# Optimization experiments

Hardware: AMD Instinct MI355X
Metric: run time of the kernel (lower is better)

The kernel has to match this reference:

```python
import jax, jax.numpy as jnp
import numpy as np

B, N, F_NODE, F_EDGE, F_G = 2, 512, 128, 16, 128
MID, OUT = 128, 128


def _linear_params(key, fan_in, fan_out):
    kw, kb = jax.random.split(key)
    scale = 1.0 / np.sqrt(fan_in)
    W = jax.random.normal(kw, (fan_in, fan_out), dtype=jnp.float32) * scale
    b = jnp.zeros((fan_out,), dtype=jnp.float32)
    return W, b


def setup_inputs() -> dict:
    key = jax.random.key(0)
    ks = jax.random.split(key, 12)
    features = jax.random.normal(ks[0], (B, N, F_NODE), dtype=jnp.float32)
    e_features = jax.random.normal(ks[1], (B, N, N, F_EDGE), dtype=jnp.float32)
    g_features = jax.random.normal(ks[2], (B, F_G), dtype=jnp.float32)
    adj = jax.random.randint(ks[3], (B, N, N), 0, 2).astype(jnp.float32)
    W1, b1 = _linear_params(ks[4], F_NODE, MID)
    W2, b2 = _linear_params(ks[5], F_NODE, MID)
    We, be = _linear_params(ks[6], F_EDGE, MID)
    Wg, bg = _linear_params(ks[7], F_G, MID)
    Wo1, bo1 = _linear_params(ks[8], F_NODE, OUT)
    Wo2, bo2 = _linear_params(ks[9], MID, OUT)
    return dict(features=features, e_features=e_features, g_features=g_features,
                adj=adj, W1=W1, b1=b1, W2=W2, b2=b2, We=We, be=be, Wg=Wg, bg=bg,
                Wo1=Wo1, bo1=bo1, Wo2=Wo2, bo2=bo2)


def reference(features, e_features, g_features, adj,
              W1, b1, W2, b2, We, be, Wg, bg, Wo1, bo1, Wo2, bo2):
    # Linear projections (haiku Linear = xW + b)
    msg_1 = jnp.einsum('bnf,fm->bnm', features, W1) + b1      # (b,n,mid)
    msg_2 = jnp.einsum('bnf,fm->bnm', features, W2) + b2      # (b,n,mid)
    msg_e = jnp.einsum('bije,em->bijm', e_features, We) + be  # (b,n,n,mid)
    msg_g = jnp.einsum('bg,gm->bm', g_features, Wg) + bg      # (b,mid)
    # All-pairs broadcast sum: (b,n,n,mid)
    msgs = (msg_1[:, None, :, :] + msg_2[:, :, None, :]
            + msg_e + msg_g[:, None, None, :])
    # Masked max reduction over axis=1 (default reduction=jnp.max)
    msgs = jnp.max(msgs * adj[..., None], axis=1)             # (b,n,mid)
    h_1 = jnp.einsum('bnf,fo->bno', features, Wo1) + bo1
    h_2 = jnp.einsum('bnm,mo->bno', msgs, Wo2) + bo2
    return h_1 + h_2
```

## Files before the change

### kernel.cpp

```cpp
#include <hip/hip_runtime.h>
#include <hip/hip_bf16.h>
#include <math.h>

#define B_   2
#define N_   512
#define FN   128
#define FE   16
#define MID_ 128

typedef __attribute__((ext_vector_type(8)))  short short8_t;
typedef __attribute__((ext_vector_type(16))) float f32x16;

__device__ __forceinline__ short f2bf(float f) {
    __bf16 h = (__bf16)f;
    return __builtin_bit_cast(short, h);
}

__global__ __launch_bounds__(64) void kA(
    const float* __restrict__ feat, const float* __restrict__ gfeat,
    const float* __restrict__ W1, const float* __restrict__ b1,
    const float* __restrict__ W2, const float* __restrict__ be,
    const float* __restrict__ Wg, const float* __restrict__ bg,
    const float* __restrict__ Wo1,
    float* __restrict__ msg1c, float* __restrict__ msg2, float* __restrict__ h1,
    float* __restrict__ msgg)
{
    const int bid = blockIdx.x;
    const int t   = threadIdx.x;

    if (bid >= 384) {
        const int b = bid - 384;
        const float* gb = gfeat + b * FN;
        #pragma unroll
        for (int half = 0; half < 2; ++half) {
            const int m = t + 64 * half;
            float mg = b1[m] + be[m] + bg[m];
            for (int k0 = 0; k0 < FN; k0 += 16) {
                float wv[16];
                #pragma unroll
                for (int u = 0; u < 16; ++u) wv[u] = Wg[(k0 + u) * MID_ + m];
                #pragma unroll
                for (int u = 0; u < 16; ++u) mg += gb[k0 + u] * wv[u];
            }
            msgg[b * MID_ + m] = mg;
        }
        return;
    }

    const int bb  = bid / 192;
    const int rem = bid - bb * 192;
    const int nt  = rem / 12;
    const int ct  = rem - nt * 12;
    const int w   = ct >> 2;
    const int c0  = (ct & 3) * 32;
    const int n0  = nt * 32;
    const int g   = t >> 5, lm = t & 31;

    const float* Ws  = (w == 0) ? W1    : (w == 1) ? W2   : Wo1;
    float*       dst = (w == 0) ? msg1c : (w == 1) ? msg2 : h1;

    short8_t Af[8];
    #pragma unroll
    for (int ks = 0; ks < 8; ++ks) {
        const float* ap = feat + (size_t)(bb * N_ + n0 + lm) * FN + ks * 16 + 8 * g;
        const float4 a0 = *(const float4*)ap;
        const float4 a1 = *(const float4*)(ap + 4);
        short8_t A;
        A[0] = f2bf(a0.x); A[1] = f2bf(a0.y); A[2] = f2bf(a0.z); A[3] = f2bf(a0.w);
        A[4] = f2bf(a1.x); A[5] = f2bf(a1.y); A[6] = f2bf(a1.z); A[7] = f2bf(a1.w);
        Af[ks] = A;
    }
    short8_t Bfr[8];
    #pragma unroll
    for (int ks = 0; ks < 8; ++ks) {
        short8_t Bv;
        #pragma unroll
        for (int j = 0; j < 8; ++j)
            Bv[j] = f2bf(Ws[(size_t)(ks * 16 + 8 * g + j) * MID_ + c0 + lm]);
        Bfr[ks] = Bv;
    }

    f32x16 acc;
    #pragma unroll
    for (int r = 0; r < 16; ++r) acc[r] = 0.0f;
    #pragma unroll
    for (int ks = 0; ks < 8; ++ks)
        acc = __builtin_amdgcn_mfma_f32_32x32x16_bf16(Af[ks], Bfr[ks], acc, 0, 0, 0);

    #pragma unroll
    for (int r = 0; r < 16; ++r) {
        const int row = (r & 3) + 8 * (r >> 2) + 4 * g;
        dst[(size_t)(bb * N_ + n0 + row) * MID_ + c0 + lm] = acc[r];
    }
}

__global__ __launch_bounds__(512, 4) void kB(
    const float* __restrict__ ef, const float* __restrict__ adj,
    const float* __restrict__ We, const float* __restrict__ b2,
    const float* __restrict__ msg1c, const float* __restrict__ msg2,
    const float* __restrict__ msgg,
    float* __restrict__ part)
{
    __shared__ float    m2l[32 * MID_];
    __shared__ float    mtile[4][32 * 32];
    __shared__ unsigned madj[32];
    __shared__ float    anyzf[32];

    const int bid = blockIdx.x;
    const int b   = bid >> 8;
    const int jt  = (bid >> 4) & 15;
    const int ic  = bid & 15;
    const int j0  = jt * 32, i0 = ic * 32;
    const int t    = threadIdx.x;
    const int lane = t & 63, wid = t >> 6;
    const int mt   = wid & 3, ih = wid >> 2;
    const int g    = lane >> 5, lm = lane & 31;

    {
        const float4* src = (const float4*)(msg2 + (size_t)(b * N_ + i0) * MID_);
        ((float4*)m2l)[t]       = src[t];
        ((float4*)m2l)[t + 512] = src[t + 512];
    }
    #pragma unroll
    for (int p = 0; p < 2; ++p) {
        const int i_l = wid * 4 + 2 * p + g;
        const float av = adj[(size_t)(b * N_ + i0 + i_l) * N_ + j0 + lm];
        const unsigned long long bal = __ballot(av != 0.0f);
        if (lane == 0)  madj[wid * 4 + 2 * p]     = (unsigned)bal;
        if (lane == 32) madj[wid * 4 + 2 * p + 1] = (unsigned)(bal >> 32);
    }
    short8_t Bf;
    #pragma unroll
    for (int jj = 0; jj < 8; ++jj)
        Bf[jj] = f2bf(We[(8 * g + jj) * MID_ + mt * 32 + lm]);
    const float b2v = b2[mt * 32 + lm];

    f32x16 accm;
    #pragma unroll
    for (int r = 0; r < 16; ++r) accm[r] = -INFINITY;

    __syncthreads();

    if (t < 32) {
        unsigned ao = 0xFFFFFFFFu;
        #pragma unroll
        for (int i2 = 0; i2 < 32; ++i2) ao &= madj[i2];
        anyzf[t] = ((ao >> t) & 1u) ? -INFINITY : 0.0f;
    }

    const float* efr = ef + (((size_t)(b * N_ + i0 + ih * 16)) * N_ + j0 + lm) * FE + 8 * g;
    #pragma unroll 2
    for (int ii = 0; ii < 16; ++ii) {
        const int i_l = ih * 16 + ii;
        const float4 ea = *(const float4*)efr;
        const float4 eb = *(const float4*)(efr + 4);
        efr += (size_t)N_ * FE;
        short8_t Af;
        Af[0] = f2bf(ea.x); Af[1] = f2bf(ea.y); Af[2] = f2bf(ea.z); Af[3] = f2bf(ea.w);
        Af[4] = f2bf(eb.x); Af[5] = f2bf(eb.y); Af[6] = f2bf(eb.z); Af[7] = f2bf(eb.w);

        const unsigned vmg = madj[i_l] >> (4 * g);
        const float m2v = m2l[i_l * MID_ + mt * 32 + lm] + b2v;
        f32x16 C;
        #pragma unroll
        for (int r = 0; r < 16; ++r) {
            const int cr = (r & 3) + 8 * (r >> 2);
            C[r] = (vmg & (1u << cr)) ? m2v : -INFINITY;
        }
        const f32x16 S = __builtin_amdgcn_mfma_f32_32x32x16_bf16(Af, Bf, C, 0, 0, 0);
        #pragma unroll
        for (int r = 0; r < 16; ++r) accm[r] = fmaxf(accm[r], S[r]);
    }

    if (ih == 1) {
        #pragma unroll
        for (int r = 0; r < 16; ++r) {
            const int jrow = (r & 3) + 8 * (r >> 2) + 4 * g;
            mtile[mt][jrow * 32 + lm] = accm[r];
        }
    }
    __syncthreads();
    float* ftile = m2l;
    if (ih == 0) {
        #pragma unroll
        for (int r = 0; r < 16; ++r) {
            const int jrow = (r & 3) + 8 * (r >> 2) + 4 * g;
            ftile[jrow * MID_ + mt * 32 + lm] = fmaxf(accm[r], mtile[mt][jrow * 32 + lm]);
        }
    }
    __syncthreads();

    {
        const int jrow = t >> 4, m0 = (t & 15) * 8;
        const float az = anyzf[jrow];
        const float*  c1  = msg1c + (size_t)(b * N_ + j0 + jrow) * MID_ + m0;
        const float*  gg  = msgg + b * MID_ + m0;
        float*        dst = part  + ((size_t)(ic * 2 + b) * N_ + j0 + jrow) * MID_ + m0;
        const float*  tl  = &ftile[jrow * MID_ + m0];
        const float4 c1a = *(const float4*)c1;
        const float4 c1b = *(const float4*)(c1 + 4);
        const float4 g1a = *(const float4*)gg;
        const float4 g1b = *(const float4*)(gg + 4);
        float4 o0, o1;
        o0.x = fmaxf(tl[0] + c1a.x + g1a.x, az);
        o0.y = fmaxf(tl[1] + c1a.y + g1a.y, az);
        o0.z = fmaxf(tl[2] + c1a.z + g1a.z, az);
        o0.w = fmaxf(tl[3] + c1a.w + g1a.w, az);
        o1.x = fmaxf(tl[4] + c1b.x + g1b.x, az);
        o1.y = fmaxf(tl[5] + c1b.y + g1b.y, az);
        o1.z = fmaxf(tl[6] + c1b.z + g1b.z, az);
        o1.w = fmaxf(tl[7] + c1b.w + g1b.w, az);
        *(float4*)dst       = o0;
        *(float4*)(dst + 4) = o1;
    }
}

__global__ __launch_bounds__(256, 2) void kC(
    const float* __restrict__ part, const float* __restrict__ h1,
    const float* __restrict__ Wo2, const float* __restrict__ bo1,
    const float* __restrict__ bo2,
    float* __restrict__ out)
{
    __shared__ float ms[2 * MID_];
    const int bid = blockIdx.x;
    const int b   = bid >> 8;
    const int j0  = (bid & 255) * 2;
    const int t   = threadIdx.x;
    const int r   = t >> 7, m = t & 127;
    const size_t base = ((size_t)b * N_ + j0 + r) * MID_ + m;

    float u = -INFINITY;
    #pragma unroll
    for (int icc = 0; icc < 16; ++icc)
        u = fmaxf(u, part[(size_t)icc * 2 * N_ * MID_ + base]);
    ms[r * MID_ + m] = u;
    __syncthreads();

    float acc = h1[base] + bo1[m] + bo2[m];
    for (int k0 = 0; k0 < MID_; k0 += 8) {
        float wv[8];
        #pragma unroll
        for (int uu = 0; uu < 8; ++uu) wv[uu] = Wo2[(k0 + uu) * MID_ + m];
        #pragma unroll
        for (int uu = 0; uu < 8; ++uu) acc += ms[r * MID_ + k0 + uu] * wv[uu];
    }
    out[base] = acc;
}

extern "C" void kernel_launch(void* const* d_in, const int* in_sizes, int n_in,
                              void* d_out, int out_size, void* d_ws, size_t ws_size,
                              hipStream_t stream)
{
    const float* feat = (const float*)d_in[0];
    const float* ef   = (const float*)d_in[1];
    const float* gf   = (const float*)d_in[2];
    const float* adj  = (const float*)d_in[3];
    const float* W1   = (const float*)d_in[4];
    const float* b1   = (const float*)d_in[5];
    const float* W2   = (const float*)d_in[6];
    const float* b2   = (const float*)d_in[7];
    const float* We   = (const float*)d_in[8];
    const float* be   = (const float*)d_in[9];
    const float* Wg   = (const float*)d_in[10];
    const float* bg   = (const float*)d_in[11];
    const float* Wo1  = (const float*)d_in[12];
    const float* bo1  = (const float*)d_in[13];
    const float* Wo2  = (const float*)d_in[14];
    const float* bo2  = (const float*)d_in[15];
    float* out = (float*)d_out;

    float* ws    = (float*)d_ws;
    float* msg1c = ws;
    float* msg2  = ws + 131072;
    float* h1    = ws + 262144;
    float* part  = ws + 393216;
    float* msgg  = ws + 393216 + 2097152;

    hipLaunchKernelGGL(kA, dim3(386), dim3(64), 0, stream,
        feat, gf, W1, b1, W2, be, Wg, bg, Wo1, msg1c, msg2, h1, msgg);
    hipLaunchKernelGGL(kB, dim3(512), dim3(512), 0, stream,
        ef, adj, We, b2, msg1c, msg2, msgg, part);
    hipLaunchKernelGGL(kC, dim3(512), dim3(256), 0, stream,
        part, h1, Wo2, bo1, bo2, out);
}
```

Baseline: 30.07 us.

## Replace per-chunk partial buffer with atomicMax on order-preserving encoded floats

Instead of writing 16 partial max tiles to workspace and reducing them in kC, kB now combines results with atomicMax on an order-preserving unsigned encoding of the floats. kA zero-initialises the encoded buffer, and kC just decodes a single value. The edge-feature loop is also software-pipelined, loading the next row before processing the current one. This removes about 8MB of partial-buffer writes and reads, but adds many global atomics with contention across the 16 i-chunks, and the per-element stores are no longer vectorised.

```diff
diff --git a/kernel.cpp b/kernel.cpp
--- a/kernel.cpp
+++ b/kernel.cpp
@@ -14,6 +14,14 @@
 __device__ __forceinline__ short f2bf(float f) {
     __bf16 h = (__bf16)f;
     return __builtin_bit_cast(short, h);
+}
+__device__ __forceinline__ unsigned enc_f32(float f) {
+    unsigned u = __float_as_uint(f);
+    return u ^ (0x80000000u | (unsigned)((int)u >> 31));
+}
+__device__ __forceinline__ float dec_f32(unsigned u) {
+    unsigned m = (u & 0x80000000u) ? 0x80000000u : 0xFFFFFFFFu;
+    return __uint_as_float(u ^ m);
 }
 
 __global__ __launch_bounds__(64) void kA(
@@ -23,10 +31,21 @@
     const float* __restrict__ Wg, const float* __restrict__ bg,
     const float* __restrict__ Wo1,
     float* __restrict__ msg1c, float* __restrict__ msg2, float* __restrict__ h1,
-    float* __restrict__ msgg)
+    float* __restrict__ msgg, unsigned* __restrict__ msgs_enc)
 {
     const int bid = blockIdx.x;
     const int t   = threadIdx.x;
+
+    {
+        const int s0 = bid * 86;
+        #pragma unroll
+        for (int q = 0; q < 2; ++q) {
+            const int rel = t + 64 * q;
+            const int slot = s0 + rel;
+            if (rel < 86 && slot < 32768)
+                ((uint4*)msgs_enc)[slot] = make_uint4(0u, 0u, 0u, 0u);
+        }
+    }
 
     if (bid >= 384) {
         const int b = bid - 384;
@@ -99,7 +118,7 @@
     const float* __restrict__ We, const float* __restrict__ b2,
     const float* __restrict__ msg1c, const float* __restrict__ msg2,
     const float* __restrict__ msgg,
-    float* __restrict__ part)
+    unsigned* __restrict__ msgs_enc)
 {
     __shared__ float    m2l[32 * MID_];
     __shared__ float    mtile[4][32 * 32];
@@ -149,12 +168,18 @@
     }
 
     const float* efr = ef + (((size_t)(b * N_ + i0 + ih * 16)) * N_ + j0 + lm) * FE + 8 * g;
-    #pragma unroll 2
+    float4 ea = *(const float4*)efr;
+    float4 eb = *(const float4*)(efr + 4);
+    efr += (size_t)N_ * FE;
+    #pragma unroll
     for (int ii = 0; ii < 16; ++ii) {
+        float4 na, nb;
+        if (ii < 15) {
+            na = *(const float4*)efr;
+            nb = *(const float4*)(efr + 4);
+            efr += (size_t)N_ * FE;
+        }
         const int i_l = ih * 16 + ii;
-        const float4 ea = *(const float4*)efr;
-        const float4 eb = *(const float4*)(efr + 4);
-        efr += (size_t)N_ * FE;
         short8_t Af;
         Af[0] = f2bf(ea.x); Af[1] = f2bf(ea.y); Af[2] = f2bf(ea.z); Af[3] = f2bf(ea.w);
         Af[4] = f2bf(eb.x); Af[5] = f2bf(eb.y); Af[6] = f2bf(eb.z); Af[7] = f2bf(eb.w);
@@ -170,6 +195,7 @@
         const f32x16 S = __builtin_amdgcn_mfma_f32_32x32x16_bf16(Af, Bf, C, 0, 0, 0);
         #pragma unroll
         for (int r = 0; r < 16; ++r) accm[r] = fmaxf(accm[r], S[r]);
+        ea = na; eb = nb;
     }
 
     if (ih == 1) {
@@ -193,30 +219,20 @@
     {
         const int jrow = t >> 4, m0 = (t & 15) * 8;
         const float az = anyzf[jrow];
-        const float*  c1  = msg1c + (size_t)(b * N_ + j0 + jrow) * MID_ + m0;
-        const float*  gg  = msgg + b * MID_ + m0;
-        float*        dst = part  + ((size_t)(ic * 2 + b) * N_ + j0 + jrow) * MID_ + m0;
-        const float*  tl  = &ftile[jrow * MID_ + m0];
-        const float4 c1a = *(const float4*)c1;
-        const float4 c1b = *(const float4*)(c1 + 4);
-        const float4 g1a = *(const float4*)gg;
-        const float4 g1b = *(const float4*)(gg + 4);
-        float4 o0, o1;
-        o0.x = fmaxf(tl[0] + c1a.x + g1a.x, az);
-        o0.y = fmaxf(tl[1] + c1a.y + g1a.y, az);
-        o0.z = fmaxf(tl[2] + c1a.z + g1a.z, az);
-        o0.w = fmaxf(tl[3] + c1a.w + g1a.w, az);
-        o1.x = fmaxf(tl[4] + c1b.x + g1b.x, az);
-        o1.y = fmaxf(tl[5] + c1b.y + g1b.y, az);
-        o1.z = fmaxf(tl[6] + c1b.z + g1b.z, az);
-        o1.w = fmaxf(tl[7] + c1b.w + g1b.w, az);
-        *(float4*)dst       = o0;
-        *(float4*)(dst + 4) = o1;
+        const float*  c1 = msg1c + (size_t)(b * N_ + j0 + jrow) * MID_ + m0;
+        const float*  gg = msgg + b * MID_ + m0;
+        const float*  tl = &ftile[jrow * MID_ + m0];
+        unsigned* dst = msgs_enc + (size_t)(b * N_ + j0 + jrow) * MID_ + m0;
+        #pragma unroll
+        for (int q = 0; q < 8; ++q) {
+            const float v = fmaxf(tl[q] + c1[q] + gg[q], az);
+            atomicMax(dst + q, enc_f32(v));
+        }
     }
 }
 
 __global__ __launch_bounds__(256, 2) void kC(
-    const float* __restrict__ part, const float* __restrict__ h1,
+    const unsigned* __restrict__ msgs_enc, const float* __restrict__ h1,
     const float* __restrict__ Wo2, const float* __restrict__ bo1,
     const float* __restrict__ bo2,
     float* __restrict__ out)
@@ -229,11 +245,7 @@
     const int r   = t >> 7, m = t & 127;
     const size_t base = ((size_t)b * N_ + j0 + r) * MID_ + m;
 
-    float u = -INFINITY;
-    #pragma unroll
-    for (int icc = 0; icc < 16; ++icc)
-        u = fmaxf(u, part[(size_t)icc * 2 * N_ * MID_ + base]);
-    ms[r * MID_ + m] = u;
+    ms[r * MID_ + m] = dec_f32(msgs_enc[base]);
     __syncthreads();
 
     float acc = h1[base] + bo1[m] + bo2[m];
@@ -269,17 +281,17 @@
     const float* bo2  = (const float*)d_in[15];
     float* out = (float*)d_out;
 
-    float* ws    = (float*)d_ws;
-    float* msg1c = ws;
-    float* msg2  = ws + 131072;
-    float* h1    = ws + 262144;
-    float* part  = ws + 393216;
-    float* msgg  = ws + 393216 + 2097152;
+    float*    ws       = (float*)d_ws;
+    float*    msg1c    = ws;
+    float*    msg2     = ws + 131072;
+    float*    h1       = ws + 262144;
+    unsigned* msgs_enc = (unsigned*)(ws + 393216);
+    float*    msgg     = ws + 393216 + 131072;
 
     hipLaunchKernelGGL(kA, dim3(386), dim3(64), 0, stream,
-        feat, gf, W1, b1, W2, be, Wg, bg, Wo1, msg1c, msg2, h1, msgg);
+        feat, gf, W1, b1, W2, be, Wg, bg, Wo1, msg1c, msg2, h1, msgg, msgs_enc);
     hipLaunchKernelGGL(kB, dim3(512), dim3(512), 0, stream,
-        ef, adj, We, b2, msg1c, msg2, msgg, part);
+        ef, adj, We, b2, msg1c, msg2, msgg, msgs_enc);
     hipLaunchKernelGGL(kC, dim3(512), dim3(256), 0, stream,
-        part, h1, Wo2, bo1, bo2, out);
-}
+        msgs_enc, h1, Wo2, bo1, bo2, out);
+}
```

After: 75.50 us. 151% more time.

## Split waves over i into four groups each computing two M-tiles with shared A

Applied to the files above, without the earlier changes.

Changes the wave decomposition in kB: each wave now covers 64 output channels (two MFMA N-tiles) over 8 i-rows instead of 32 channels over 16 i-rows. The edge-feature load and bf16 conversion for A is reused across two MFMAs, halving per-wave global ef loads and conversions. In exchange it needs a two-level shared-memory tree reduction with an extra barrier, doubles the shared tile, and raises register pressure from two accumulators.

```diff
diff --git a/kernel.cpp b/kernel.cpp
--- a/kernel.cpp
+++ b/kernel.cpp
@@ -102,7 +102,7 @@
     float* __restrict__ part)
 {
     __shared__ float    m2l[32 * MID_];
-    __shared__ float    mtile[4][32 * 32];
+    __shared__ float    T[2][2][32 * 64];
     __shared__ unsigned madj[32];
     __shared__ float    anyzf[32];
 
@@ -113,7 +113,8 @@
     const int j0  = jt * 32, i0 = ic * 32;
     const int t    = threadIdx.x;
     const int lane = t & 63, wid = t >> 6;
-    const int mt   = wid & 3, ih = wid >> 2;
+    const int mtg  = wid >> 2;
+    const int ig   = wid & 3;
     const int g    = lane >> 5, lm = lane & 31;
 
     {
@@ -129,15 +130,18 @@
         if (lane == 0)  madj[wid * 4 + 2 * p]     = (unsigned)bal;
         if (lane == 32) madj[wid * 4 + 2 * p + 1] = (unsigned)(bal >> 32);
     }
-    short8_t Bf;
-    #pragma unroll
-    for (int jj = 0; jj < 8; ++jj)
-        Bf[jj] = f2bf(We[(8 * g + jj) * MID_ + mt * 32 + lm]);
-    const float b2v = b2[mt * 32 + lm];
-
-    f32x16 accm;
-    #pragma unroll
-    for (int r = 0; r < 16; ++r) accm[r] = -INFINITY;
+    short8_t Bf0, Bf1;
+    #pragma unroll
+    for (int jj = 0; jj < 8; ++jj) {
+        Bf0[jj] = f2bf(We[(8 * g + jj) * MID_ + mtg * 64 + lm]);
+        Bf1[jj] = f2bf(We[(8 * g + jj) * MID_ + mtg * 64 + 32 + lm]);
+    }
+    const float b2v0 = b2[mtg * 64 + lm];
+    const float b2v1 = b2[mtg * 64 + 32 + lm];
+
+    f32x16 accm0, accm1;
+    #pragma unroll
+    for (int r = 0; r < 16; ++r) { accm0[r] = -INFINITY; accm1[r] = -INFINITY; }
 
     __syncthreads();
 
@@ -148,10 +152,10 @@
         anyzf[t] = ((ao >> t) & 1u) ? -INFINITY : 0.0f;
     }
 
-    const float* efr = ef + (((size_t)(b * N_ + i0 + ih * 16)) * N_ + j0 + lm) * FE + 8 * g;
+    const float* efr = ef + (((size_t)(b * N_ + i0 + ig * 8)) * N_ + j0 + lm) * FE + 8 * g;
     #pragma unroll 2
-    for (int ii = 0; ii < 16; ++ii) {
-        const int i_l = ih * 16 + ii;
+    for (int ii = 0; ii < 8; ++ii) {
+        const int i_l = ig * 8 + ii;
         const float4 ea = *(const float4*)efr;
         const float4 eb = *(const float4*)(efr + 4);
         efr += (size_t)N_ * FE;
@@ -160,32 +164,69 @@
         Af[4] = f2bf(eb.x); Af[5] = f2bf(eb.y); Af[6] = f2bf(eb.z); Af[7] = f2bf(eb.w);
 
         const unsigned vmg = madj[i_l] >> (4 * g);
-        const float m2v = m2l[i_l * MID_ + mt * 32 + lm] + b2v;
-        f32x16 C;
+        const float m2v0 = m2l[i_l * MID_ + mtg * 64 + lm]      + b2v0;
+        const float m2v1 = m2l[i_l * MID_ + mtg * 64 + 32 + lm] + b2v1;
+        f32x16 msk;
         #pragma unroll
         for (int r = 0; r < 16; ++r) {
             const int cr = (r & 3) + 8 * (r >> 2);
-            C[r] = (vmg & (1u << cr)) ? m2v : -INFINITY;
-        }
-        const f32x16 S = __builtin_amdgcn_mfma_f32_32x32x16_bf16(Af, Bf, C, 0, 0, 0);
-        #pragma unroll
-        for (int r = 0; r < 16; ++r) accm[r] = fmaxf(accm[r], S[r]);
-    }
-
-    if (ih == 1) {
+            msk[r] = (vmg & (1u << cr)) ? 0.0f : -INFINITY;
+        }
+        f32x16 C0;
+        #pragma unroll
+        for (int r = 0; r < 16; ++r) C0[r] = m2v0 + msk[r];
+        const f32x16 S0 = __builtin_amdgcn_mfma_f32_32x32x16_bf16(Af, Bf0, C0, 0, 0, 0);
+        #pragma unroll
+        for (int r = 0; r < 16; ++r) accm0[r] = fmaxf(accm0[r], S0[r]);
+
+        f32x16 C1;
+        #pragma unroll
+        for (int r = 0; r < 16; ++r) C1[r] = m2v1 + msk[r];
+        const f32x16 S1 = __builtin_amdgcn_mfma_f32_32x32x16_bf16(Af, Bf1, C1, 0, 0, 0);
+        #pragma unroll
+        for (int r = 0; r < 16; ++r) accm1[r] = fmaxf(accm1[r], S1[r]);
+    }
+
+    __syncthreads();
+    if (ig & 1) {
+        float* Tw = T[mtg][ig >> 1];
         #pragma unroll
         for (int r = 0; r < 16; ++r) {
             const int jrow = (r & 3) + 8 * (r >> 2) + 4 * g;
-            mtile[mt][jrow * 32 + lm] = accm[r];
+            Tw[jrow * 64 + lm]      = accm0[r];
+            Tw[jrow * 64 + 32 + lm] = accm1[r];
+        }
+    }
+    __syncthreads();
+    if (!(ig & 1)) {
+        const float* Tr = T[mtg][ig >> 1];
+        #pragma unroll
+        for (int r = 0; r < 16; ++r) {
+            const int jrow = (r & 3) + 8 * (r >> 2) + 4 * g;
+            accm0[r] = fmaxf(accm0[r], Tr[jrow * 64 + lm]);
+            accm1[r] = fmaxf(accm1[r], Tr[jrow * 64 + 32 + lm]);
+        }
+    }
+    if (ig == 2) {
+        float* Tw = T[mtg][1];
+        #pragma unroll
+        for (int r = 0; r < 16; ++r) {
+            const int jrow = (r & 3) + 8 * (r >> 2) + 4 * g;
+            Tw[jrow * 64 + lm]      = accm0[r];
+            Tw[jrow * 64 + 32 + lm] = accm1[r];
         }
     }
     __syncthreads();
     float* ftile = m2l;
-    if (ih == 0) {
+    if (ig == 0) {
+        const float* Tr = T[mtg][1];
         #pragma unroll
         for (int r = 0; r < 16; ++r) {
             const int jrow = (r & 3) + 8 * (r >> 2) + 4 * g;
-            ftile[jrow * MID_ + mt * 32 + lm] = fmaxf(accm[r], mtile[mt][jrow * 32 + lm]);
+            const float v0 = fmaxf(accm0[r], Tr[jrow * 64 + lm]);
+            const float v1 = fmaxf(accm1[r], Tr[jrow * 64 + 32 + lm]);
+            ftile[jrow * MID_ + mtg * 64 + lm]      = v0;
+            ftile[jrow * MID_ + mtg * 64 + 32 + lm] = v1;
         }
     }
     __syncthreads();
```

Measured after the change: 30.15 us. About the same (+0.3%).

## Split kB into smaller i-chunks with register-only reduction, dropping shared memory

Applied to the files above, without the earlier changes.

kB now uses 256-thread blocks over 16-row i-chunks (1024 blocks), so each wave covers all 16 rows of its chunk. The adjacency masks and the any-zero mask live in registers, msg2 is read directly from global memory, and the result is written straight from the accumulators. This removes all shared memory, the block barriers and the cross-wave max merge. In exchange the partial buffer doubles in size, kC must reduce 32 partials instead of 16, and the global stores are less coalesced.

```diff
diff --git a/kernel.cpp b/kernel.cpp
--- a/kernel.cpp
+++ b/kernel.cpp
@@ -94,41 +94,35 @@
     }
 }
 
-__global__ __launch_bounds__(512, 4) void kB(
+__global__ __launch_bounds__(256, 4) void kB(
     const float* __restrict__ ef, const float* __restrict__ adj,
     const float* __restrict__ We, const float* __restrict__ b2,
     const float* __restrict__ msg1c, const float* __restrict__ msg2,
     const float* __restrict__ msgg,
     float* __restrict__ part)
 {
-    __shared__ float    m2l[32 * MID_];
-    __shared__ float    mtile[4][32 * 32];
-    __shared__ unsigned madj[32];
-    __shared__ float    anyzf[32];
-
     const int bid = blockIdx.x;
-    const int b   = bid >> 8;
-    const int jt  = (bid >> 4) & 15;
-    const int ic  = bid & 15;
-    const int j0  = jt * 32, i0 = ic * 32;
+    const int b   = bid >> 9;
+    const int jt  = (bid >> 5) & 15;
+    const int ic  = bid & 31;
+    const int j0  = jt * 32, i0 = ic * 16;
     const int t    = threadIdx.x;
-    const int lane = t & 63, wid = t >> 6;
-    const int mt   = wid & 3, ih = wid >> 2;
+    const int lane = t & 63, mt = t >> 6;
     const int g    = lane >> 5, lm = lane & 31;
 
-    {
-        const float4* src = (const float4*)(msg2 + (size_t)(b * N_ + i0) * MID_);
-        ((float4*)m2l)[t]       = src[t];
-        ((float4*)m2l)[t + 512] = src[t + 512];
-    }
-    #pragma unroll
-    for (int p = 0; p < 2; ++p) {
-        const int i_l = wid * 4 + 2 * p + g;
+    unsigned m[16];
+    #pragma unroll
+    for (int p = 0; p < 8; ++p) {
+        const int i_l = 2 * p + g;
         const float av = adj[(size_t)(b * N_ + i0 + i_l) * N_ + j0 + lm];
         const unsigned long long bal = __ballot(av != 0.0f);
-        if (lane == 0)  madj[wid * 4 + 2 * p]     = (unsigned)bal;
-        if (lane == 32) madj[wid * 4 + 2 * p + 1] = (unsigned)(bal >> 32);
-    }
+        m[2 * p]     = (unsigned)bal;
+        m[2 * p + 1] = (unsigned)(bal >> 32);
+    }
+    unsigned andm = 0xFFFFFFFFu;
+    #pragma unroll
+    for (int i = 0; i < 16; ++i) andm &= m[i];
+
     short8_t Bf;
     #pragma unroll
     for (int jj = 0; jj < 8; ++jj)
@@ -139,28 +133,20 @@
     #pragma unroll
     for (int r = 0; r < 16; ++r) accm[r] = -INFINITY;
 
-    __syncthreads();
-
-    if (t < 32) {
-        unsigned ao = 0xFFFFFFFFu;
-        #pragma unroll
-        for (int i2 = 0; i2 < 32; ++i2) ao &= madj[i2];
-        anyzf[t] = ((ao >> t) & 1u) ? -INFINITY : 0.0f;
-    }
-
-    const float* efr = ef + (((size_t)(b * N_ + i0 + ih * 16)) * N_ + j0 + lm) * FE + 8 * g;
-    #pragma unroll 2
+    const float* efr = ef + ((size_t)(b * N_ + i0) * N_ + j0 + lm) * FE + 8 * g;
+    const float* m2p = msg2 + (size_t)(b * N_ + i0) * MID_ + mt * 32 + lm;
+    #pragma unroll
     for (int ii = 0; ii < 16; ++ii) {
-        const int i_l = ih * 16 + ii;
         const float4 ea = *(const float4*)efr;
         const float4 eb = *(const float4*)(efr + 4);
         efr += (size_t)N_ * FE;
+        const float m2v = *m2p + b2v;
+        m2p += MID_;
         short8_t Af;
         Af[0] = f2bf(ea.x); Af[1] = f2bf(ea.y); Af[2] = f2bf(ea.z); Af[3] = f2bf(ea.w);
         Af[4] = f2bf(eb.x); Af[5] = f2bf(eb.y); Af[6] = f2bf(eb.z); Af[7] = f2bf(eb.w);
 
-        const unsigned vmg = madj[i_l] >> (4 * g);
-        const float m2v = m2l[i_l * MID_ + mt * 32 + lm] + b2v;
+        const unsigned vmg = m[ii] >> (4 * g);
         f32x16 C;
         #pragma unroll
         for (int r = 0; r < 16; ++r) {
@@ -172,46 +158,14 @@
         for (int r = 0; r < 16; ++r) accm[r] = fmaxf(accm[r], S[r]);
     }
 
-    if (ih == 1) {
-        #pragma unroll
-        for (int r = 0; r < 16; ++r) {
-            const int jrow = (r & 3) + 8 * (r >> 2) + 4 * g;
-            mtile[mt][jrow * 32 + lm] = accm[r];
-        }
-    }
-    __syncthreads();
-    float* ftile = m2l;
-    if (ih == 0) {
-        #pragma unroll
-        for (int r = 0; r < 16; ++r) {
-            const int jrow = (r & 3) + 8 * (r >> 2) + 4 * g;
-            ftile[jrow * MID_ + mt * 32 + lm] = fmaxf(accm[r], mtile[mt][jrow * 32 + lm]);
-        }
-    }
-    __syncthreads();
-
-    {
-        const int jrow = t >> 4, m0 = (t & 15) * 8;
-        const float az = anyzf[jrow];
-        const float*  c1  = msg1c + (size_t)(b * N_ + j0 + jrow) * MID_ + m0;
-        const float*  gg  = msgg + b * MID_ + m0;
-        float*        dst = part  + ((size_t)(ic * 2 + b) * N_ + j0 + jrow) * MID_ + m0;
-        const float*  tl  = &ftile[jrow * MID_ + m0];
-        const float4 c1a = *(const float4*)c1;
-        const float4 c1b = *(const float4*)(c1 + 4);
-        const float4 g1a = *(const float4*)gg;
-        const float4 g1b = *(const float4*)(gg + 4);
-        float4 o0, o1;
-        o0.x = fmaxf(tl[0] + c1a.x + g1a.x, az);
-        o0.y = fmaxf(tl[1] + c1a.y + g1a.y, az);
-        o0.z = fmaxf(tl[2] + c1a.z + g1a.z, az);
-        o0.w = fmaxf(tl[3] + c1a.w + g1a.w, az);
-        o1.x = fmaxf(tl[4] + c1b.x + g1b.x, az);
-        o1.y = fmaxf(tl[5] + c1b.y + g1b.y, az);
-        o1.z = fmaxf(tl[6] + c1b.z + g1b.z, az);
-        o1.w = fmaxf(tl[7] + c1b.w + g1b.w, az);
-        *(float4*)dst       = o0;
-        *(float4*)(dst + 4) = o1;
+    const float ggv = msgg[b * MID_ + mt * 32 + lm];
+    #pragma unroll
+    for (int r = 0; r < 16; ++r) {
+        const int jrow = (r & 3) + 8 * (r >> 2) + 4 * g;
+        const float az = ((andm >> jrow) & 1u) ? -INFINITY : 0.0f;
+        const float c1v = msg1c[(size_t)(b * N_ + j0 + jrow) * MID_ + mt * 32 + lm];
+        const float v = fmaxf(accm[r] + c1v + ggv, az);
+        part[((size_t)(ic * 2 + b) * N_ + j0 + jrow) * MID_ + mt * 32 + lm] = v;
     }
 }
 
@@ -231,7 +185,7 @@
 
     float u = -INFINITY;
     #pragma unroll
-    for (int icc = 0; icc < 16; ++icc)
+    for (int icc = 0; icc < 32; ++icc)
         u = fmaxf(u, part[(size_t)icc * 2 * N_ * MID_ + base]);
     ms[r * MID_ + m] = u;
     __syncthreads();
@@ -274,11 +228,11 @@
     float* msg2  = ws + 131072;
     float* h1    = ws + 262144;
     float* part  = ws + 393216;
-    float* msgg  = ws + 393216 + 2097152;
+    float* msgg  = ws + 393216 + 4194304;
 
     hipLaunchKernelGGL(kA, dim3(386), dim3(64), 0, stream,
         feat, gf, W1, b1, W2, be, Wg, bg, Wo1, msg1c, msg2, h1, msgg);
-    hipLaunchKernelGGL(kB, dim3(512), dim3(512), 0, stream,
+    hipLaunchKernelGGL(kB, dim3(1024), dim3(256), 0, stream,
         ef, adj, We, b2, msg1c, msg2, msgg, part);
     hipLaunchKernelGGL(kC, dim3(512), dim3(256), 0, stream,
         part, h1, Wo2, bo1, bo2, out);
```

After: 31.10 us. +3.4%, slower.
